# Kernel tuning notes

Measured on AMD Instinct MI355X. Metric: run time of the kernel, lower is better.

The kernel has to match this reference:

```python
import jax, jax.numpy as jnp
import numpy as np

V = 256        # vocab (bytes)
DM = 1024      # d_model
NL = 8         # num layers
N = 16         # d_state
K = 4          # d_conv
E = 2 * DM     # d_inner (expand=2)
R = DM // 16   # dt_rank = 64
EPS = 1e-5
B, T = 1, 1024


def setup_inputs() -> dict:
    key = jax.random.key(0)
    ks = jax.random.split(key, 10)
    s = lambda i, shape, scale=0.02: jax.random.normal(ks[i], shape, jnp.float32) * scale
    A_init = jnp.log(jnp.tile(jnp.arange(1, N + 1, dtype=jnp.float32), (NL, E, 1)))
    return {
        "input_ids": jax.random.randint(ks[0], (B, T), 0, V),
        "embed": s(1, (V, DM)),
        "Wxz": s(2, (NL, DM, 2 * E)),            # in_proj (no bias)
        "conv_w": s(3, (NL, E, K), 0.1),          # depthwise causal conv
        "conv_b": jnp.zeros((NL, E), jnp.float32),
        "Wx": s(4, (NL, E, R + 2 * N)),           # x_proj -> dt, B, C
        "Wdt": s(5, (NL, R, E), 0.1),             # dt_proj
        "dt_bias": jnp.full((NL, E), -4.6, jnp.float32),  # softplus(-4.6) ~ 0.01
        "A_log": A_init,                          # A = -exp(A_log), S4D-real init
        "D": jnp.ones((NL, E), jnp.float32),      # skip connection
        "Wout": s(6, (NL, E, DM)),                # out_proj (no bias)
        "norm_w": jnp.ones((NL, DM), jnp.float32),
        "final_norm_w": jnp.ones((DM,), jnp.float32),
        "lm_head_w": s(7, (DM, V)),               # lm_head (no bias)
    }


def rmsnorm(x, w):
    return x * jax.lax.rsqrt(jnp.mean(x * x, axis=-1, keepdims=True) + EPS) * w


def selective_scan(x, dt, A, Bm, Cm, Dp):
    # x, dt: [B,T,E]; A: [E,N]; Bm, Cm: [B,T,N]; Dp: [E]
    dA = jnp.exp(dt[..., None] * A)                              # [B,T,E,N]
    dBx = dt[..., None] * Bm[:, :, None, :] * x[..., None]       # [B,T,E,N]

    def step(h, inp):
        dA_t, dBx_t, C_t = inp                                   # [B,E,N],[B,E,N],[B,N]
        h = dA_t * h + dBx_t
        y = jnp.einsum('ben,bn->be', h, C_t)
        return h, y

    h0 = jnp.zeros((x.shape[0], E, N), x.dtype)
    _, ys = jax.lax.scan(step, h0, (dA.transpose(1, 0, 2, 3),
                                    dBx.transpose(1, 0, 2, 3),
                                    Cm.transpose(1, 0, 2)))
    return ys.transpose(1, 0, 2) + Dp * x                        # [B,T,E]


def mamba_layer(h, p):
    Wxz, cw, cb, Wx, Wdt, dtb, A_log, Dp, Wout, nw = p
    res = h
    u = rmsnorm(h, nw)
    xz = u @ Wxz                                                 # [B,T,2E]
    x, z = jnp.split(xz, 2, axis=-1)
    # causal depthwise conv over time
    xc = jax.lax.conv_general_dilated(x.transpose(0, 2, 1), cw[:, None, :],
                                      (1,), [(K - 1, 0)], feature_group_count=E)
    x = jax.nn.silu(xc.transpose(0, 2, 1) + cb)                  # [B,T,E]
    xdbl = x @ Wx                                                # [B,T,R+2N]
    dt = jax.nn.softplus(xdbl[..., :R] @ Wdt + dtb)              # [B,T,E]
    Bm = xdbl[..., R:R + N]
    Cm = xdbl[..., R + N:]
    A = -jnp.exp(A_log)                                          # [E,N]
    y = selective_scan(x, dt, A, Bm, Cm, Dp)
    y = y * jax.nn.silu(z)
    return res + y @ Wout, None


def reference(input_ids, embed, Wxz, conv_w, conv_b, Wx, Wdt, dt_bias, A_log, D,
              Wout, norm_w, final_norm_w, lm_head_w):
    h = embed[input_ids]                                         # [B,T,DM]
    h, _ = jax.lax.scan(mamba_layer, h,
                        (Wxz, conv_w, conv_b, Wx, Wdt, dt_bias, A_log, D, Wout, norm_w))
    h = rmsnorm(h, final_norm_w)
    return h @ lm_head_w                                         # logits [B,T,V]
```

## Files before the change

kernel.cpp:

```cpp
#include <hip/hip_runtime.h>
#include <hip/hip_bf16.h>

#define DM_   1024
#define NLAY  8
#define NST   16
#define KCONV 4
#define EE    2048
#define E2    4096
#define RNK   64
#define SEQ   1024
#define NXD   96
#define VOC   256
#define EPS_  1e-5f
#define NCH   32
#define CLEN  32

typedef __attribute__((ext_vector_type(8))) short bf16x8;
typedef __attribute__((ext_vector_type(4))) float f32x4;
typedef __hip_bfloat16 bf16;

__device__ __forceinline__ float sigmoidf_(float x){ return 1.f/(1.f+__expf(-x)); }
__device__ __forceinline__ float siluf_(float x){ return x*sigmoidf_(x); }
__device__ __forceinline__ float softplusf_(float x){ return (x>15.f)?x:log1pf(__expf(x)); }

__device__ __forceinline__ void gld_lds16(const short* g, short* lds_uniform){
  __builtin_amdgcn_global_load_lds(
      (const __attribute__((address_space(1))) unsigned int*)(const void*)g,
      (__attribute__((address_space(3))) unsigned int*)(void*)lds_uniform,
      16, 0, 0);
}

__global__ void k_embed(const int* __restrict__ ids, const float* __restrict__ emb,
                        float* __restrict__ h){
  int t = blockIdx.x;
  int v = ids[t];
  const float* src = emb + (size_t)v*DM_;
  float* dst = h + (size_t)t*DM_;
  for (int i = threadIdx.x; i < DM_; i += 256) dst[i] = src[i];
}

__global__ void k_transpose_bf16(const float* __restrict__ in, bf16* __restrict__ out,
                                 int rows, int cols, long in_stride, long out_stride){
  __shared__ float tile[32][33];
  const float* inp = in + (size_t)blockIdx.z * in_stride;
  bf16* outp = out + (size_t)blockIdx.z * out_stride;
  int c0 = blockIdx.x*32, r0 = blockIdx.y*32;
  int tx = threadIdx.x, ty = threadIdx.y;
#pragma unroll
  for (int j = 0; j < 4; j++)
    tile[ty + j*8][tx] = inp[(size_t)(r0 + ty + j*8)*cols + c0 + tx];
  __syncthreads();
#pragma unroll
  for (int j = 0; j < 4; j++)
    outp[(size_t)(c0 + ty + j*8)*rows + r0 + tx] = __float2bfloat16(tile[tx][ty + j*8]);
}

__global__ void k_rmsnorm_bf16(const float* __restrict__ h, const float* __restrict__ w,
                               bf16* __restrict__ u){
  int t = blockIdx.x;
  const float* hp = h + (size_t)t*DM_;
  float ss = 0.f;
  for (int i = threadIdx.x; i < DM_; i += 256){ float v = hp[i]; ss += v*v; }
#pragma unroll
  for (int o = 32; o > 0; o >>= 1) ss += __shfl_down(ss, o, 64);
  __shared__ float red[4];
  if ((threadIdx.x & 63) == 0) red[threadIdx.x >> 6] = ss;
  __syncthreads();
  float tot = red[0]+red[1]+red[2]+red[3];
  float sc = rsqrtf(tot*(1.f/DM_) + EPS_);
  bf16* up = u + (size_t)t*DM_;
  for (int i = threadIdx.x; i < DM_; i += 256)
    up[i] = __float2bfloat16(hp[i]*sc*w[i]);
}

template<int BM, int BN, int NWM, int NWN, int MODE>
__global__ __launch_bounds__(256,1) void k_gemm(
    const short* __restrict__ A, const short* __restrict__ Bt, float* __restrict__ C,
    int M, int N, int K, int Ksplit,
    const float* __restrict__ bias, const float* __restrict__ res)
{
  constexpr int BK = 64;
  constexpr int WM = BM/NWM, WN = BN/NWN;
  constexpr int MT = WM/16, NT = WN/16;
  constexpr int ABY = BM*BK*2, BBY = BN*BK*2;
  constexpr int AISS = ABY/4096, BISS = BBY/4096;
  __shared__ __align__(16) short As[2][BM*BK];
  __shared__ __align__(16) short Bs[2][BN*BK];
  int tid = threadIdx.x, lane = tid & 63, wave = tid >> 6;
  int wr = wave / NWN, wc = wave % NWN;
  int m0 = blockIdx.x * BM, n0 = blockIdx.y * BN;
  int lrow = lane & 15, lq = lane >> 4;
  int wbase = (tid & ~63) * 16;

  int kbeg = blockIdx.z * Ksplit;
  int nk = Ksplit / BK;

  f32x4 acc[MT][NT];
#pragma unroll
  for (int i = 0; i < MT; i++)
#pragma unroll
    for (int j = 0; j < NT; j++) acc[i][j] = (f32x4){0.f,0.f,0.f,0.f};

  auto stage = [&](int k0, int buf){
#pragma unroll
    for (int i = 0; i < AISS; i++){
      int off = i*4096 + tid*16;
      int row = off >> 7;
      int kc  = ((off >> 4) & 7) ^ (row & 7);
      gld_lds16(A + (size_t)(m0+row)*K + k0 + kc*8,
                As[buf] + ((i*4096 + wbase) >> 1));
    }
#pragma unroll
    for (int i = 0; i < BISS; i++){
      int off = i*4096 + tid*16;
      int row = off >> 7;
      int kc  = ((off >> 4) & 7) ^ (row & 7);
      gld_lds16(Bt + (size_t)(n0+row)*K + k0 + kc*8,
                Bs[buf] + ((i*4096 + wbase) >> 1));
    }
  };

  stage(kbeg, 0);
  __syncthreads();
  for (int it = 0; it < nk; it++){
    int cur = it & 1;
    if (it + 1 < nk) stage(kbeg + (it+1)*BK, cur ^ 1);
#pragma unroll
    for (int s = 0; s < 2; s++){
      bf16x8 af[MT], bfr[NT];
#pragma unroll
      for (int mt = 0; mt < MT; mt++){
        int row = wr*WM + mt*16 + lrow;
        int cc = (s*4 + lq) ^ (row & 7);
        af[mt] = *(const bf16x8*)(As[cur] + row*BK + cc*8);
      }
#pragma unroll
      for (int nt = 0; nt < NT; nt++){
        int row = wc*WN + nt*16 + lrow;
        int cc = (s*4 + lq) ^ (row & 7);
        bfr[nt] = *(const bf16x8*)(Bs[cur] + row*BK + cc*8);
      }
#pragma unroll
      for (int mt = 0; mt < MT; mt++)
#pragma unroll
        for (int nt = 0; nt < NT; nt++)
          acc[mt][nt] = __builtin_amdgcn_mfma_f32_16x16x32_bf16(af[mt], bfr[nt], acc[mt][nt], 0,0,0);
    }
    __syncthreads();
  }

#pragma unroll
  for (int mt = 0; mt < MT; mt++){
    int row = m0 + wr*WM + mt*16 + lq*4;
#pragma unroll
    for (int nt = 0; nt < NT; nt++){
      int col = n0 + wc*WN + nt*16 + lrow;
#pragma unroll
      for (int r = 0; r < 4; r++){
        float v = acc[mt][nt][r];
        size_t idx = (size_t)(row + r)*N + col;
        if (MODE == 1){ C[idx] = softplusf_(v + bias[col]); }
        else if (MODE == 3){
          if (res && blockIdx.z == 0) v += res[idx];
          atomicAdd(&C[idx], v);
        } else { C[idx] = v; }
      }
    }
  }
}

__global__ void k_conv_silu(const float* __restrict__ xz, const float* __restrict__ cw,
                            const float* __restrict__ cb, float* __restrict__ xact,
                            bf16* __restrict__ xbf){
  int t = blockIdx.y;
  int e = blockIdx.x*256 + threadIdx.x;
  float4 w4 = *(const float4*)(cw + (size_t)e*4);
  float acc = cb[e];
  if (t >= 3){
    acc += xz[(size_t)(t-3)*E2 + e]*w4.x + xz[(size_t)(t-2)*E2 + e]*w4.y
         + xz[(size_t)(t-1)*E2 + e]*w4.z + xz[(size_t)t*E2 + e]*w4.w;
  } else {
    const float* wp = (const float*)&w4;
#pragma unroll
    for (int k = 0; k < 4; k++){ int tt = t-3+k; if (tt >= 0) acc += xz[(size_t)tt*E2 + e]*wp[k]; }
  }
  float xv = siluf_(acc);
  xact[(size_t)t*EE + e] = xv;
  xbf[(size_t)t*EE + e] = __float2bfloat16(xv);
}

__global__ void k_cast_dtproj(const float* __restrict__ xdbl, bf16* __restrict__ out){
  int t = blockIdx.x;
  out[(size_t)t*RNK + threadIdx.x] = __float2bfloat16(xdbl[(size_t)t*NXD + threadIdx.x]);
}

__global__ void k_scanA(const float* __restrict__ dt, const float* __restrict__ x,
                        const float* __restrict__ xdbl, const float* __restrict__ Alog,
                        float* __restrict__ S, float* __restrict__ dtsum){
  int e = blockIdx.x*256 + threadIdx.x;
  int c = blockIdx.y;
  int t0 = c*CLEN;
  float Ae[NST];
#pragma unroll
  for (int n = 0; n < NST; n++) Ae[n] = -__expf(Alog[(size_t)e*NST + n]);
  __shared__ float Bsm[CLEN][NST];
  for (int i = threadIdx.x; i < CLEN*NST; i += 256)
    Bsm[i>>4][i&15] = xdbl[(size_t)(t0 + (i>>4))*NXD + RNK + (i&15)];
  __syncthreads();
  float h[NST];
#pragma unroll
  for (int n = 0; n < NST; n++) h[n] = 0.f;
  float ds = 0.f;
  for (int tt = 0; tt < CLEN; tt++){
    float dtv = dt[(size_t)(t0+tt)*EE + e];
    float xv  = x[(size_t)(t0+tt)*EE + e];
    ds += dtv;
    float sx = dtv * xv;
#pragma unroll
    for (int n = 0; n < NST; n++)
      h[n] = __expf(dtv*Ae[n])*h[n] + sx*Bsm[tt][n];
  }
  float* Sp = S + ((size_t)c*EE + e)*NST;
#pragma unroll
  for (int n = 0; n < NST; n++) Sp[n] = h[n];
  dtsum[(size_t)c*EE + e] = ds;
}

__global__ void k_scanB(const float* __restrict__ S, const float* __restrict__ dtsum,
                        const float* __restrict__ Alog, float* __restrict__ hinit){
  int idx = blockIdx.x*256 + threadIdx.x;
  float An = -__expf(Alog[idx]);
  int e = idx >> 4;
  float h = 0.f;
  for (int c = 0; c < NCH; c++){
    hinit[(size_t)c*EE*NST + idx] = h;
    h = __expf(dtsum[(size_t)c*EE + e]*An)*h + S[(size_t)c*EE*NST + idx];
  }
}

__global__ void k_scanC(const float* __restrict__ dt, const float* __restrict__ x,
                        const float* __restrict__ xdbl, const float* __restrict__ Alog,
                        const float* __restrict__ Dp, const float* __restrict__ hinit,
                        const float* __restrict__ xz, bf16* __restrict__ ybf){
  int e = blockIdx.x*256 + threadIdx.x;
  int c = blockIdx.y;
  int t0 = c*CLEN;
  float Ae[NST];
#pragma unroll
  for (int n = 0; n < NST; n++) Ae[n] = -__expf(Alog[(size_t)e*NST + n]);
  __shared__ float Bsm[CLEN][NST], Csm[CLEN][NST];
  for (int i = threadIdx.x; i < CLEN*NST; i += 256){
    int tt = i>>4, n = i&15;
    Bsm[tt][n] = xdbl[(size_t)(t0+tt)*NXD + RNK + n];
    Csm[tt][n] = xdbl[(size_t)(t0+tt)*NXD + RNK + NST + n];
  }
  __syncthreads();
  float h[NST];
  const float* hp = hinit + ((size_t)c*EE + e)*NST;
#pragma unroll
  for (int n = 0; n < NST; n++) h[n] = hp[n];
  float Dv = Dp[e];
  for (int tt = 0; tt < CLEN; tt++){
    float dtv = dt[(size_t)(t0+tt)*EE + e];
    float xv  = x[(size_t)(t0+tt)*EE + e];
    float sx = dtv*xv;
    float y = Dv*xv;
#pragma unroll
    for (int n = 0; n < NST; n++){
      h[n] = __expf(dtv*Ae[n])*h[n] + sx*Bsm[tt][n];
      y += h[n]*Csm[tt][n];
    }
    float zv = xz[(size_t)(t0+tt)*E2 + EE + e];
    y *= zv*sigmoidf_(zv);
    ybf[(size_t)(t0+tt)*EE + e] = __float2bfloat16(y);
  }
}

extern "C" void kernel_launch(void* const* d_in, const int* in_sizes, int n_in,
                              void* d_out, int out_size, void* d_ws, size_t ws_size,
                              hipStream_t stream)
{
  const int*   ids  = (const int*)d_in[0];
  const float* emb  = (const float*)d_in[1];
  const float* Wxz  = (const float*)d_in[2];
  const float* cw   = (const float*)d_in[3];
  const float* cb   = (const float*)d_in[4];
  const float* Wx   = (const float*)d_in[5];
  const float* Wdt  = (const float*)d_in[6];
  const float* dtb  = (const float*)d_in[7];
  const float* Alog = (const float*)d_in[8];
  const float* Dp   = (const float*)d_in[9];
  const float* Wout = (const float*)d_in[10];
  const float* nw   = (const float*)d_in[11];
  const float* fnw  = (const float*)d_in[12];
  const float* lmw  = (const float*)d_in[13];

  char* p = (char*)d_ws;
  auto alloc = [&](size_t bytes){ void* r = (void*)p; p += (bytes + 255) & ~(size_t)255; return r; };
  bf16* wxz_bf  = (bf16*)alloc((size_t)NLAY*E2*DM_*2);
  bf16* wout_bf = (bf16*)alloc((size_t)NLAY*DM_*EE*2);
  bf16* wx_bf   = (bf16*)alloc((size_t)NLAY*NXD*EE*2);
  bf16* wdt_bf  = (bf16*)alloc((size_t)NLAY*EE*RNK*2);
  bf16* lm_bf   = (bf16*)alloc((size_t)VOC*DM_*2);
  float* hA     = (float*)alloc((size_t)SEQ*DM_*4);
  float* hB     = (float*)alloc((size_t)SEQ*DM_*4);
  bf16* u_bf    = (bf16*)alloc((size_t)SEQ*DM_*2);
  float* xzb    = (float*)alloc((size_t)SEQ*E2*4);
  float* xact   = (float*)alloc((size_t)SEQ*EE*4);
  bf16* x_bf    = (bf16*)alloc((size_t)SEQ*EE*2);
  float* xdbl   = (float*)alloc((size_t)SEQ*NXD*4);
  bf16* xd64    = (bf16*)alloc((size_t)SEQ*RNK*2);
  float* dtbuf  = (float*)alloc((size_t)SEQ*EE*4);
  float* Sbuf   = (float*)alloc((size_t)NCH*EE*NST*4);
  float* dtsum  = (float*)alloc((size_t)NCH*EE*4);
  float* hinit  = (float*)alloc((size_t)NCH*EE*NST*4);
  bf16* y_bf    = (bf16*)alloc((size_t)SEQ*EE*2);

  k_transpose_bf16<<<dim3(E2/32, DM_/32, NLAY), dim3(32,8), 0, stream>>>(Wxz, wxz_bf, DM_, E2, (long)DM_*E2, (long)E2*DM_);
  k_transpose_bf16<<<dim3(DM_/32, EE/32, NLAY), dim3(32,8), 0, stream>>>(Wout, wout_bf, EE, DM_, (long)EE*DM_, (long)DM_*EE);
  k_transpose_bf16<<<dim3(NXD/32, EE/32, NLAY), dim3(32,8), 0, stream>>>(Wx, wx_bf, EE, NXD, (long)EE*NXD, (long)NXD*EE);
  k_transpose_bf16<<<dim3(EE/32, RNK/32, NLAY), dim3(32,8), 0, stream>>>(Wdt, wdt_bf, RNK, EE, (long)RNK*EE, (long)EE*RNK);
  k_transpose_bf16<<<dim3(VOC/32, DM_/32, 1), dim3(32,8), 0, stream>>>(lmw, lm_bf, DM_, VOC, 0, 0);

  k_embed<<<SEQ, 256, 0, stream>>>(ids, emb, hA);

  float* hcur = hA; float* hnxt = hB;
  for (int l = 0; l < NLAY; l++){
    hipMemsetAsync(hnxt, 0, (size_t)SEQ*DM_*4, stream);
    k_rmsnorm_bf16<<<SEQ, 256, 0, stream>>>(hcur, nw + (size_t)l*DM_, u_bf);
    k_gemm<128,128,2,2,0><<<dim3(SEQ/128, E2/128, 1), 256, 0, stream>>>(
        (const short*)u_bf, (const short*)(wxz_bf + (size_t)l*E2*DM_), xzb,
        SEQ, E2, DM_, DM_, nullptr, nullptr);
    k_conv_silu<<<dim3(EE/256, SEQ), 256, 0, stream>>>(
        xzb, cw + (size_t)l*EE*KCONV, cb + (size_t)l*EE, xact, x_bf);
    hipMemsetAsync(xdbl, 0, (size_t)SEQ*NXD*4, stream);
    k_gemm<64,96,2,2,3><<<dim3(SEQ/64, 1, 8), 256, 0, stream>>>(
        (const short*)x_bf, (const short*)(wx_bf + (size_t)l*NXD*EE), xdbl,
        SEQ, NXD, EE, EE/8, nullptr, nullptr);
    k_cast_dtproj<<<SEQ, RNK, 0, stream>>>(xdbl, xd64);
    k_gemm<64,64,2,2,1><<<dim3(SEQ/64, EE/64, 1), 256, 0, stream>>>(
        (const short*)xd64, (const short*)(wdt_bf + (size_t)l*EE*RNK), dtbuf,
        SEQ, EE, RNK, RNK, dtb + (size_t)l*EE, nullptr);
    k_scanA<<<dim3(EE/256, NCH), 256, 0, stream>>>(
        dtbuf, xact, xdbl, Alog + (size_t)l*EE*NST, Sbuf, dtsum);
    k_scanB<<<dim3(EE*NST/256), 256, 0, stream>>>(Sbuf, dtsum, Alog + (size_t)l*EE*NST, hinit);
    k_scanC<<<dim3(EE/256, NCH), 256, 0, stream>>>(
        dtbuf, xact, xdbl, Alog + (size_t)l*EE*NST, Dp + (size_t)l*EE, hinit, xzb, y_bf);
    k_gemm<64,64,2,2,3><<<dim3(SEQ/64, DM_/64, 2), 256, 0, stream>>>(
        (const short*)y_bf, (const short*)(wout_bf + (size_t)l*DM_*EE), hnxt,
        SEQ, DM_, EE, EE/2, nullptr, hcur);
    float* tmp = hcur; hcur = hnxt; hnxt = tmp;
  }
  k_rmsnorm_bf16<<<SEQ, 256, 0, stream>>>(hcur, fnw, u_bf);
  hipMemsetAsync(d_out, 0, (size_t)SEQ*VOC*4, stream);
  k_gemm<64,64,2,2,3><<<dim3(SEQ/64, VOC/64, 4), 256, 0, stream>>>(
      (const short*)u_bf, (const short*)lm_bf, (float*)d_out,
      SEQ, VOC, DM_, DM_/4, nullptr, nullptr);
}
```

Measured before the change: 1.303 ms.

## Replace split-K atomics with slab reductions fused into rmsnorm and embed

Split-K GEMMs now write per-split partial slabs instead of using atomicAdd into memset buffers. The residual add and the slab reduction are folded into the next layer's rmsnorm, which also takes over the embedding gather. Separate reduce kernels sum the x_proj and lm_head partials, and the x_proj reduce also emits the bf16 dt input. Tile shapes change (in_proj 128x64, x_proj 32x96) and the one-block-per-CU launch bound is dropped. This removes memsets, atomics and a few launches at the cost of extra slab memory traffic.

```diff
diff --git a/kernel.cpp b/kernel.cpp
--- a/kernel.cpp
+++ b/kernel.cpp
@@ -30,15 +30,6 @@
       16, 0, 0);
 }
 
-__global__ void k_embed(const int* __restrict__ ids, const float* __restrict__ emb,
-                        float* __restrict__ h){
-  int t = blockIdx.x;
-  int v = ids[t];
-  const float* src = emb + (size_t)v*DM_;
-  float* dst = h + (size_t)t*DM_;
-  for (int i = threadIdx.x; i < DM_; i += 256) dst[i] = src[i];
-}
-
 __global__ void k_transpose_bf16(const float* __restrict__ in, bf16* __restrict__ out,
                                  int rows, int cols, long in_stride, long out_stride){
   __shared__ float tile[32][33];
@@ -55,12 +46,23 @@
     outp[(size_t)(c0 + ty + j*8)*rows + r0 + tx] = __float2bfloat16(tile[tx][ty + j*8]);
 }
 
-__global__ void k_rmsnorm_bf16(const float* __restrict__ h, const float* __restrict__ w,
+__global__ void k_rmsnorm_fuse(const int* __restrict__ ids, const float* __restrict__ emb,
+                               float* __restrict__ h, const float* __restrict__ s0,
+                               const float* __restrict__ s1, const float* __restrict__ w,
                                bf16* __restrict__ u){
   int t = blockIdx.x;
-  const float* hp = h + (size_t)t*DM_;
+  float* hp = h + (size_t)t*DM_;
+  float v[4];
   float ss = 0.f;
-  for (int i = threadIdx.x; i < DM_; i += 256){ float v = hp[i]; ss += v*v; }
+#pragma unroll
+  for (int j = 0; j < 4; j++){
+    int i = threadIdx.x + j*256;
+    float x;
+    if (ids){ x = emb[(size_t)ids[t]*DM_ + i]; hp[i] = x; }
+    else if (s0){ x = hp[i] + s0[(size_t)t*DM_ + i] + s1[(size_t)t*DM_ + i]; hp[i] = x; }
+    else { x = hp[i]; }
+    v[j] = x; ss += x*x;
+  }
 #pragma unroll
   for (int o = 32; o > 0; o >>= 1) ss += __shfl_down(ss, o, 64);
   __shared__ float red[4];
@@ -69,15 +71,17 @@
   float tot = red[0]+red[1]+red[2]+red[3];
   float sc = rsqrtf(tot*(1.f/DM_) + EPS_);
   bf16* up = u + (size_t)t*DM_;
-  for (int i = threadIdx.x; i < DM_; i += 256)
-    up[i] = __float2bfloat16(hp[i]*sc*w[i]);
+#pragma unroll
+  for (int j = 0; j < 4; j++){
+    int i = threadIdx.x + j*256;
+    up[i] = __float2bfloat16(v[j]*sc*w[i]);
+  }
 }
 
 template<int BM, int BN, int NWM, int NWN, int MODE>
-__global__ __launch_bounds__(256,1) void k_gemm(
+__global__ __launch_bounds__(256) void k_gemm(
     const short* __restrict__ A, const short* __restrict__ Bt, float* __restrict__ C,
-    int M, int N, int K, int Ksplit,
-    const float* __restrict__ bias, const float* __restrict__ res)
+    int M, int N, int K, int Ksplit, const float* __restrict__ bias)
 {
   constexpr int BK = 64;
   constexpr int WM = BM/NWM, WN = BN/NWN;
@@ -149,6 +153,7 @@
     __syncthreads();
   }
 
+  size_t slab = (MODE == 4) ? (size_t)blockIdx.z * M * N : 0;
 #pragma unroll
   for (int mt = 0; mt < MT; mt++){
     int row = m0 + wr*WM + mt*16 + lq*4;
@@ -158,12 +163,9 @@
 #pragma unroll
       for (int r = 0; r < 4; r++){
         float v = acc[mt][nt][r];
-        size_t idx = (size_t)(row + r)*N + col;
-        if (MODE == 1){ C[idx] = softplusf_(v + bias[col]); }
-        else if (MODE == 3){
-          if (res && blockIdx.z == 0) v += res[idx];
-          atomicAdd(&C[idx], v);
-        } else { C[idx] = v; }
+        size_t idx = slab + (size_t)(row + r)*N + col;
+        if (MODE == 1) C[idx] = softplusf_(v + bias[col]);
+        else C[idx] = v;
       }
     }
   }
@@ -189,9 +191,23 @@
   xbf[(size_t)t*EE + e] = __float2bfloat16(xv);
 }
 
-__global__ void k_cast_dtproj(const float* __restrict__ xdbl, bf16* __restrict__ out){
-  int t = blockIdx.x;
-  out[(size_t)t*RNK + threadIdx.x] = __float2bfloat16(xdbl[(size_t)t*NXD + threadIdx.x]);
+__global__ void k_reduce_xdbl(const float* __restrict__ s, float* __restrict__ out,
+                              bf16* __restrict__ out64){
+  int i = blockIdx.x*256 + threadIdx.x;
+  float v = 0.f;
+#pragma unroll
+  for (int c = 0; c < 8; c++) v += s[(size_t)c*SEQ*NXD + i];
+  out[i] = v;
+  int t = i / NXD, cc = i - t*NXD;
+  if (cc < RNK) out64[(size_t)t*RNK + cc] = __float2bfloat16(v);
+}
+
+__global__ void k_reduce_lm(const float* __restrict__ s, float* __restrict__ out){
+  int i = blockIdx.x*256 + threadIdx.x;
+  float v = 0.f;
+#pragma unroll
+  for (int c = 0; c < 4; c++) v += s[(size_t)c*SEQ*VOC + i];
+  out[i] = v;
 }
 
 __global__ void k_scanA(const float* __restrict__ dt, const float* __restrict__ x,
@@ -302,12 +318,13 @@
   bf16* wx_bf   = (bf16*)alloc((size_t)NLAY*NXD*EE*2);
   bf16* wdt_bf  = (bf16*)alloc((size_t)NLAY*EE*RNK*2);
   bf16* lm_bf   = (bf16*)alloc((size_t)VOC*DM_*2);
-  float* hA     = (float*)alloc((size_t)SEQ*DM_*4);
-  float* hB     = (float*)alloc((size_t)SEQ*DM_*4);
+  float* h      = (float*)alloc((size_t)SEQ*DM_*4);
+  float* hslab  = (float*)alloc((size_t)2*SEQ*DM_*4);
   bf16* u_bf    = (bf16*)alloc((size_t)SEQ*DM_*2);
   float* xzb    = (float*)alloc((size_t)SEQ*E2*4);
   float* xact   = (float*)alloc((size_t)SEQ*EE*4);
   bf16* x_bf    = (bf16*)alloc((size_t)SEQ*EE*2);
+  float* xdbl_s = (float*)alloc((size_t)8*SEQ*NXD*4);
   float* xdbl   = (float*)alloc((size_t)SEQ*NXD*4);
   bf16* xd64    = (bf16*)alloc((size_t)SEQ*RNK*2);
   float* dtbuf  = (float*)alloc((size_t)SEQ*EE*4);
@@ -315,6 +332,7 @@
   float* dtsum  = (float*)alloc((size_t)NCH*EE*4);
   float* hinit  = (float*)alloc((size_t)NCH*EE*NST*4);
   bf16* y_bf    = (bf16*)alloc((size_t)SEQ*EE*2);
+  float* lmslab = (float*)alloc((size_t)4*SEQ*VOC*4);
 
   k_transpose_bf16<<<dim3(E2/32, DM_/32, NLAY), dim3(32,8), 0, stream>>>(Wxz, wxz_bf, DM_, E2, (long)DM_*E2, (long)E2*DM_);
   k_transpose_bf16<<<dim3(DM_/32, EE/32, NLAY), dim3(32,8), 0, stream>>>(Wout, wout_bf, EE, DM_, (long)EE*DM_, (long)DM_*EE);
@@ -322,38 +340,36 @@
   k_transpose_bf16<<<dim3(EE/32, RNK/32, NLAY), dim3(32,8), 0, stream>>>(Wdt, wdt_bf, RNK, EE, (long)RNK*EE, (long)EE*RNK);
   k_transpose_bf16<<<dim3(VOC/32, DM_/32, 1), dim3(32,8), 0, stream>>>(lmw, lm_bf, DM_, VOC, 0, 0);
 
-  k_embed<<<SEQ, 256, 0, stream>>>(ids, emb, hA);
-
-  float* hcur = hA; float* hnxt = hB;
   for (int l = 0; l < NLAY; l++){
-    hipMemsetAsync(hnxt, 0, (size_t)SEQ*DM_*4, stream);
-    k_rmsnorm_bf16<<<SEQ, 256, 0, stream>>>(hcur, nw + (size_t)l*DM_, u_bf);
-    k_gemm<128,128,2,2,0><<<dim3(SEQ/128, E2/128, 1), 256, 0, stream>>>(
+    k_rmsnorm_fuse<<<SEQ, 256, 0, stream>>>(
+        l == 0 ? ids : nullptr, emb, h,
+        l == 0 ? nullptr : hslab, hslab + (size_t)SEQ*DM_,
+        nw + (size_t)l*DM_, u_bf);
+    k_gemm<128,64,2,2,0><<<dim3(SEQ/128, E2/64, 1), 256, 0, stream>>>(
         (const short*)u_bf, (const short*)(wxz_bf + (size_t)l*E2*DM_), xzb,
-        SEQ, E2, DM_, DM_, nullptr, nullptr);
+        SEQ, E2, DM_, DM_, nullptr);
     k_conv_silu<<<dim3(EE/256, SEQ), 256, 0, stream>>>(
         xzb, cw + (size_t)l*EE*KCONV, cb + (size_t)l*EE, xact, x_bf);
-    hipMemsetAsync(xdbl, 0, (size_t)SEQ*NXD*4, stream);
-    k_gemm<64,96,2,2,3><<<dim3(SEQ/64, 1, 8), 256, 0, stream>>>(
-        (const short*)x_bf, (const short*)(wx_bf + (size_t)l*NXD*EE), xdbl,
-        SEQ, NXD, EE, EE/8, nullptr, nullptr);
-    k_cast_dtproj<<<SEQ, RNK, 0, stream>>>(xdbl, xd64);
+    k_gemm<32,96,2,2,4><<<dim3(SEQ/32, 1, 8), 256, 0, stream>>>(
+        (const short*)x_bf, (const short*)(wx_bf + (size_t)l*NXD*EE), xdbl_s,
+        SEQ, NXD, EE, EE/8, nullptr);
+    k_reduce_xdbl<<<SEQ*NXD/256, 256, 0, stream>>>(xdbl_s, xdbl, xd64);
     k_gemm<64,64,2,2,1><<<dim3(SEQ/64, EE/64, 1), 256, 0, stream>>>(
         (const short*)xd64, (const short*)(wdt_bf + (size_t)l*EE*RNK), dtbuf,
-        SEQ, EE, RNK, RNK, dtb + (size_t)l*EE, nullptr);
+        SEQ, EE, RNK, RNK, dtb + (size_t)l*EE);
     k_scanA<<<dim3(EE/256, NCH), 256, 0, stream>>>(
         dtbuf, xact, xdbl, Alog + (size_t)l*EE*NST, Sbuf, dtsum);
     k_scanB<<<dim3(EE*NST/256), 256, 0, stream>>>(Sbuf, dtsum, Alog + (size_t)l*EE*NST, hinit);
     k_scanC<<<dim3(EE/256, NCH), 256, 0, stream>>>(
         dtbuf, xact, xdbl, Alog + (size_t)l*EE*NST, Dp + (size_t)l*EE, hinit, xzb, y_bf);
-    k_gemm<64,64,2,2,3><<<dim3(SEQ/64, DM_/64, 2), 256, 0, stream>>>(
-        (const short*)y_bf, (const short*)(wout_bf + (size_t)l*DM_*EE), hnxt,
-        SEQ, DM_, EE, EE/2, nullptr, hcur);
-    float* tmp = hcur; hcur = hnxt; hnxt = tmp;
-  }
-  k_rmsnorm_bf16<<<SEQ, 256, 0, stream>>>(hcur, fnw, u_bf);
-  hipMemsetAsync(d_out, 0, (size_t)SEQ*VOC*4, stream);
-  k_gemm<64,64,2,2,3><<<dim3(SEQ/64, VOC/64, 4), 256, 0, stream>>>(
-      (const short*)u_bf, (const short*)lm_bf, (float*)d_out,
-      SEQ, VOC, DM_, DM_/4, nullptr, nullptr);
-}
+    k_gemm<64,64,2,2,4><<<dim3(SEQ/64, DM_/64, 2), 256, 0, stream>>>(
+        (const short*)y_bf, (const short*)(wout_bf + (size_t)l*DM_*EE), hslab,
+        SEQ, DM_, EE, EE/2, nullptr);
+  }
+  k_rmsnorm_fuse<<<SEQ, 256, 0, stream>>>(
+      nullptr, emb, h, hslab, hslab + (size_t)SEQ*DM_, fnw, u_bf);
+  k_gemm<64,64,2,2,4><<<dim3(SEQ/64, VOC/64, 4), 256, 0, stream>>>(
+      (const short*)u_bf, (const short*)lm_bf, lmslab,
+      SEQ, VOC, DM_, DM_/4, nullptr);
+  k_reduce_lm<<<SEQ*VOC/256, 256, 0, stream>>>(lmslab, (float*)d_out);
+}
```

Result: faster. 1.164 ms (-10.6%).
